# Kernel tuning notes

Hardware: AMD Instinct MI355X
Metric: run time of the kernel (lower is better)

The kernel has to match this reference:

```python
import jax, jax.numpy as jnp
import numpy as np

B, L, D_MODEL, D_MEM = 4, 8192, 512, 512
SSM_DIM = D_MODEL + D_MEM


def setup_inputs() -> dict:
    key = jax.random.key(0)
    ks = jax.random.split(key, 4)
    s = 0.02
    return {
        "x": jax.random.normal(ks[0], (B, L, D_MODEL), dtype=jnp.float32),
        "W_av": jax.random.normal(ks[1], (4 * D_MEM, D_MODEL), dtype=jnp.float32) * s,
        "b_av": jnp.zeros((4 * D_MEM,), dtype=jnp.float32),
        "W_go": jax.random.normal(ks[2], (D_MODEL, SSM_DIM), dtype=jnp.float32) * s,
        "b_go": jnp.zeros((D_MODEL,), dtype=jnp.float32),
        "W_out": jax.random.normal(ks[3], (2 * D_MODEL, D_MODEL), dtype=jnp.float32) * s,
        "b_out": jnp.zeros((2 * D_MODEL,), dtype=jnp.float32),
    }


def reference(x, W_av, b_av, W_go, b_go, W_out, b_out):
    d = D_MEM
    b = x.shape[0]
    # alpha_v = Linear(d_model -> 4*d_memory) on x[:, :-1]
    av = jnp.einsum("bld,kd->blk", x[:, :-1], W_av) + b_av
    # NRU memory update: alpha+*v+ - alpha-*v-  (all nonlins default to identity)
    ms_inp = av[..., :d] * av[..., d:2 * d] - av[..., 2 * d:3 * d] * av[..., 3 * d:4 * d]
    # associative cumsum scan along length, prefixed with zero initial memory
    ms = jnp.cumsum(ms_inp, axis=1)
    m_init = jnp.zeros((b, 1, d), dtype=x.dtype)
    ms = jnp.concatenate([m_init, ms], axis=1)  # [b, L, d_memory]
    ssm_inp = jnp.concatenate([x, ms], axis=2)  # [b, L, ssm_dim]
    # SSM sublayer (external registry module) stubbed as identity
    ssm_out = ssm_inp
    y = jnp.einsum("blk,dk->bld", ssm_out, W_go) + b_go  # gated_out
    y = jax.nn.gelu(y, approximate=False)  # activation='gelu' (torch exact erf)
    z = jnp.einsum("bld,kd->blk", y, W_out) + b_out  # [b, L, 2*d_model]
    y = z[..., :D_MODEL] * jax.nn.sigmoid(z[..., D_MODEL:])
    return y
```

## Files before the change

kernel.cpp:

```cpp
#include <hip/hip_runtime.h>
#include <hip/hip_bf16.h>
#include <math.h>

#define B_SZ 4
#define L_SZ 8192
#define DM 512
#define DMEM 512
#define M1 (B_SZ * (L_SZ - 1))
#define M2 (B_SZ * L_SZ)

typedef _Float16 h16;
typedef __attribute__((ext_vector_type(2))) _Float16 f16x2;
typedef __attribute__((ext_vector_type(8))) _Float16 f16x8;
typedef __attribute__((ext_vector_type(4))) float f32x4;

#define MFMA16(a, b, c) __builtin_amdgcn_mfma_f32_16x16x32_f16((a), (b), (c), 0, 0, 0)
#define WAVES_EU(mn, mx) __attribute__((amdgpu_waves_per_eu(mn, mx)))

__device__ __forceinline__ void gl16(const void* g, void* l) {
    __builtin_amdgcn_global_load_lds(
        (const __attribute__((address_space(1))) void*)g,
        (__attribute__((address_space(3))) void*)l, 16, 0, 0);
}

__device__ __forceinline__ f16x8 lds_frag(const h16* base, int row, int col, int key) {
    return *(const f16x8*)((const char*)base + row * 128 + ((col * 2) ^ (key << 4)));
}

__device__ __forceinline__ void xcd_remap(int& bx, int& by) {
    int gx = gridDim.x, gy = gridDim.y;
    int nwg = gx * gy;
    int lin = blockIdx.y * gx + blockIdx.x;
    int chunk = nwg >> 3;
    int l = (lin & 7) * chunk + (lin >> 3);
    by = l % gy;
    bx = l / gy;
}

__global__ __launch_bounds__(256) void prep_all(
    const float* __restrict__ x, const float* __restrict__ Wgo,
    const float* __restrict__ Wav, const float* __restrict__ Wout,
    h16* __restrict__ xh, h16* __restrict__ Wgoh,
    h16* __restrict__ Wavh, h16* __restrict__ Wouth)
{
    int i = blockIdx.x * 256 + threadIdx.x;
    const float* s;
    h16* d;
    if (i < 2097152) {
        int m = i >> 6, bb = i & 63;
        s = x + (size_t)m * 512 + bb * 8;
        d = xh + (size_t)m * 512 + (bb ^ (m & 7)) * 8;
    } else {
        int j = i - 2097152;
        if (j < 65536) {
            int r = j >> 7, bb = j & 127;
            s = Wgo + (size_t)r * 1024 + bb * 8;
            d = Wgoh + (size_t)r * 1024 + (bb ^ (r & 7)) * 8;
        } else if (j < 196608) {
            int k = j - 65536;
            int P = k >> 6, bb = k & 63;
            int by = P >> 7, lo = P & 127;
            int half = lo >> 6, g = (lo >> 4) & 3, nl = lo & 15;
            int orig = g * 512 + by * 32 + half * 16 + nl;
            s = Wav + (size_t)orig * 512 + bb * 8;
            d = Wavh + (size_t)P * 512 + (bb ^ (P & 7)) * 8;
        } else {
            int k = j - 196608;
            int P = k >> 6, bb = k & 63;
            int by = P >> 7, lo = P & 127;
            int chunk = lo >> 5, g = (lo >> 4) & 1, nl = lo & 15;
            int orig = g * 512 + by * 64 + chunk * 16 + nl;
            s = Wout + (size_t)orig * 512 + bb * 8;
            d = Wouth + (size_t)P * 512 + (bb ^ (P & 7)) * 8;
        }
    }
    const float4* sv = (const float4*)s;
    float4 v0 = sv[0], v1 = sv[1];
    float vv[8] = {v0.x, v0.y, v0.z, v0.w, v1.x, v1.y, v1.z, v1.w};
    f16x8 hh;
    #pragma unroll
    for (int j = 0; j < 8; ++j) hh[j] = (h16)vv[j];
    *(f16x8*)d = hh;
}

#define PIPE_WAIT(N) do { \
    asm volatile("s_waitcnt vmcnt(" #N ")" ::: "memory"); \
    __builtin_amdgcn_s_barrier(); \
    asm volatile("" ::: "memory"); \
} while (0)
#define PIPE_POST() do { \
    __builtin_amdgcn_s_barrier(); \
    asm volatile("" ::: "memory"); \
} while (0)

__global__ __launch_bounds__(256) WAVES_EU(4, 4) void gemm_av_mfma(
    const h16* __restrict__ xh, const h16* __restrict__ Wh,
    const float* __restrict__ bav, h16* __restrict__ ms_inp)
{
    __shared__ __align__(16) h16 As[128 * 64];
    __shared__ __align__(16) h16 Bh[128 * 64];

    int bx, by; xcd_remap(bx, by);
    const int tid = threadIdx.x, lane = tid & 63, w = tid >> 6;
    const int wm = (w & 1) * 64, wn = (w >> 1) * 64;
    const int bm = bx * 128;
    const int ln = lane & 15, ko = (lane >> 4) * 8;
    const int kb = ln & 7;
    char* lA = (char*)As; char* lH = (char*)Bh;
    const int wb = w * 1024;

    const char *aP[4], *hP[4];
    {
        const int r8 = lane >> 3, c16 = (lane & 7) * 16;
        #pragma unroll
        for (int i = 0; i < 4; ++i) {
            int row = i * 32 + w * 8 + r8;
            int mg = bm + row; if (mg > M1 - 1) mg = M1 - 1;
            size_t xr = (size_t)mg + (unsigned)mg / (L_SZ - 1);
            aP[i] = (const char*)xh + xr * (DM * 2) + c16;
            size_t br = (size_t)(by * 128 + row) * (DM * 2) + c16;
            hP[i] = (const char*)Wh + br;
        }
    }
    int ka[4];
    #pragma unroll
    for (int fm = 0; fm < 4; ++fm) {
        int m = bm + wm + fm * 16 + ln;
        int mg = m > M1 - 1 ? M1 - 1 : m;
        ka[fm] = (int)((mg + (unsigned)mg / (L_SZ - 1)) & 7);
    }

    f32x4 acc[4][4];
    #pragma unroll
    for (int i = 0; i < 4; ++i)
        #pragma unroll
        for (int j = 0; j < 4; ++j) acc[i][j] = (f32x4){0.f, 0.f, 0.f, 0.f};

#define STAGE_AV(koff) do { \
    gl16(aP[0] + (koff), lA + 0 * 4096 + wb); gl16(hP[0] + (koff), lH + 0 * 4096 + wb); \
    gl16(aP[1] + (koff), lA + 1 * 4096 + wb); gl16(hP[1] + (koff), lH + 1 * 4096 + wb); \
    gl16(aP[2] + (koff), lA + 2 * 4096 + wb); gl16(hP[2] + (koff), lH + 2 * 4096 + wb); \
    gl16(aP[3] + (koff), lA + 3 * 4096 + wb); gl16(hP[3] + (koff), lH + 3 * 4096 + wb); \
} while (0)

    STAGE_AV(0);
    for (int kt = 0; kt < 8; ++kt) {
        asm volatile("s_waitcnt vmcnt(0)" ::: "memory");
        __syncthreads();
        #pragma unroll
        for (int s = 0; s < 2; ++s) {
            const int c = s * 32 + ko;
            f16x8 a[4];
            #pragma unroll
            for (int fm = 0; fm < 4; ++fm)
                a[fm] = lds_frag(As, wm + fm * 16 + ln, c, ka[fm]);
            #pragma unroll
            for (int fn = 0; fn < 4; ++fn) {
                f16x8 vh = lds_frag(Bh, wn + fn * 16 + ln, c, kb);
                #pragma unroll
                for (int fm = 0; fm < 4; ++fm)
                    acc[fm][fn] = MFMA16(a[fm], vh, acc[fm][fn]);
            }
        }
        __syncthreads();
        if (kt < 7) STAGE_AV((kt + 1) * 128);
    }
#undef STAGE_AV

    const int lm = (lane >> 4) * 4;
    const int nn = by * 32 + (wn >> 6) * 16 + ln;
    const float b0 = bav[nn], b1 = bav[nn + 512], b2 = bav[nn + 1024], b3 = bav[nn + 1536];
    #pragma unroll
    for (int fm = 0; fm < 4; ++fm) {
        #pragma unroll
        for (int i = 0; i < 4; ++i) {
            int m = bm + wm + fm * 16 + lm + i;
            if (m < M1) {
                float a0 = acc[fm][0][i] + b0;
                float a1 = acc[fm][1][i] + b1;
                float a2 = acc[fm][2][i] + b2;
                float a3 = acc[fm][3][i] + b3;
                ms_inp[(size_t)m * DMEM + nn] = (h16)(a0 * a1 - a2 * a3);
            }
        }
    }
}

__global__ __launch_bounds__(256) void scan_pass1(
    const h16* __restrict__ ms_inp, float* __restrict__ csum)
{
    int b = blockIdx.y;
    int c = blockIdx.x * 4 + (threadIdx.x >> 6);
    int t = threadIdx.x & 63;
    int l0 = c * 32;
    int len = min(32, (L_SZ - 1) - l0);
    const h16* p = ms_inp + ((size_t)b * (L_SZ - 1) + l0) * DMEM + t * 8;
    float s[8] = {0.f, 0.f, 0.f, 0.f, 0.f, 0.f, 0.f, 0.f};
    for (int i = 0; i < len; ++i) {
        f16x8 v = *(const f16x8*)(p + (size_t)i * DMEM);
        #pragma unroll
        for (int j = 0; j < 8; ++j) s[j] += (float)v[j];
    }
    float* q = csum + ((size_t)b * 256 + c) * DMEM + t * 8;
    *(float4*)q       = make_float4(s[0], s[1], s[2], s[3]);
    *(float4*)(q + 4) = make_float4(s[4], s[5], s[6], s[7]);
}

__global__ __launch_bounds__(256) void scan_pass2(float* __restrict__ csum)
{
    __shared__ float wsum[4];
    int b = blockIdx.x >> 9, d = blockIdx.x & 511;
    int t = threadIdx.x, lane = t & 63, wv = t >> 6;
    float* p = csum + (size_t)b * 256 * DMEM + d;
    float v = p[(size_t)t * DMEM];
    #pragma unroll
    for (int off = 1; off < 64; off <<= 1) {
        float u = __shfl_up(v, off, 64);
        if (lane >= off) v += u;
    }
    if (lane == 63) wsum[wv] = v;
    __syncthreads();
    float add = 0.f;
    #pragma unroll
    for (int i = 0; i < 4; ++i) if (i < wv) add += wsum[i];
    v += add;
    float ex = __shfl_up(v, 1, 64);
    if (lane == 0) ex = add;
    p[(size_t)t * DMEM] = ex;
}

__global__ __launch_bounds__(256) void scan_pass3(
    const h16* __restrict__ ms_inp, const float* __restrict__ csum,
    h16* __restrict__ msh)
{
    int b = blockIdx.y;
    int c = blockIdx.x * 4 + (threadIdx.x >> 6);
    int t = threadIdx.x & 63;
    int l0 = c * 32;
    int len = min(32, (L_SZ - 1) - l0);
    const float* q = csum + ((size_t)b * 256 + c) * DMEM + t * 8;
    float run[8];
    #pragma unroll
    for (int j = 0; j < 8; ++j) run[j] = q[j];
    const h16* p = ms_inp + ((size_t)b * (L_SZ - 1) + l0) * DMEM + t * 8;
    if (c == 0) {
        f16x8 z = {};
        *(f16x8*)(msh + (size_t)b * L_SZ * DMEM + t * 8) = z;
    }
    for (int i = 0; i < len; ++i) {
        f16x8 v = *(const f16x8*)(p + (size_t)i * DMEM);
        f16x8 o;
        #pragma unroll
        for (int j = 0; j < 8; ++j) { run[j] += (float)v[j]; o[j] = (h16)run[j]; }
        int m = b * L_SZ + l0 + 1 + i;
        int db = t ^ (m & 7);
        *(f16x8*)(msh + (size_t)m * DMEM + db * 8) = o;
    }
}

__global__ __launch_bounds__(256) WAVES_EU(2, 2) void gemm_go_mfma(
    const h16* __restrict__ xh, const h16* __restrict__ msh,
    const h16* __restrict__ Wh,
    const float* __restrict__ bgo, h16* __restrict__ yh)
{
    __shared__ __align__(16) h16 As[2][128 * 64];
    __shared__ __align__(16) h16 Bh[2][128 * 64];

    int bx, by; xcd_remap(bx, by);
    const int tid = threadIdx.x, lane = tid & 63, w = tid >> 6;
    const int wm = (w & 1) * 64, wn = (w >> 1) * 64;
    const int bm = bx * 128, bn = by * 128;
    const int ln = lane & 15, ko = (lane >> 4) * 8;
    const int kk = ln & 7;
    const int wb = w * 1024;

    const char *xP[4], *mP[4], *hP[4];
    {
        const int r8 = lane >> 3, c16 = (lane & 7) * 16;
        #pragma unroll
        for (int i = 0; i < 4; ++i) {
            int row = i * 32 + w * 8 + r8;
            size_t ar = (size_t)(bm + row) * (DM * 2) + c16;
            xP[i] = (const char*)xh + ar;
            mP[i] = (const char*)msh + ar;
            size_t br = (size_t)(bn + row) * (2 * DM * 2) + c16;
            hP[i] = (const char*)Wh + br;
        }
    }

    f32x4 acc[4][4];
    #pragma unroll
    for (int i = 0; i < 4; ++i)
        #pragma unroll
        for (int j = 0; j < 4; ++j) acc[i][j] = (f32x4){0.f, 0.f, 0.f, 0.f};

#define STAGE_GO(tt, sel) do { \
    char* dA = (char*)As[sel]; char* dB = (char*)Bh[sel]; \
    const int bo = (tt) * 128; \
    if ((tt) < 8) { \
        const int ao = (tt) * 128; \
        gl16(xP[0] + ao, dA + 0 * 4096 + wb); gl16(hP[0] + bo, dB + 0 * 4096 + wb); \
        gl16(xP[1] + ao, dA + 1 * 4096 + wb); gl16(hP[1] + bo, dB + 1 * 4096 + wb); \
        gl16(xP[2] + ao, dA + 2 * 4096 + wb); gl16(hP[2] + bo, dB + 2 * 4096 + wb); \
        gl16(xP[3] + ao, dA + 3 * 4096 + wb); gl16(hP[3] + bo, dB + 3 * 4096 + wb); \
    } else { \
        const int ao = ((tt) - 8) * 128; \
        gl16(mP[0] + ao, dA + 0 * 4096 + wb); gl16(hP[0] + bo, dB + 0 * 4096 + wb); \
        gl16(mP[1] + ao, dA + 1 * 4096 + wb); gl16(hP[1] + bo, dB + 1 * 4096 + wb); \
        gl16(mP[2] + ao, dA + 2 * 4096 + wb); gl16(hP[2] + bo, dB + 2 * 4096 + wb); \
        gl16(mP[3] + ao, dA + 3 * 4096 + wb); gl16(hP[3] + bo, dB + 3 * 4096 + wb); \
    } \
} while (0)

    STAGE_GO(0, 0);
    STAGE_GO(1, 1);
    for (int kt = 0; kt < 16; ++kt) {
        if (kt < 15) PIPE_WAIT(8); else PIPE_WAIT(0);
        const h16* A = As[kt & 1];
        const h16* B = Bh[kt & 1];
        #pragma unroll
        for (int s = 0; s < 2; ++s) {
            const int c = s * 32 + ko;
            f16x8 a[4];
            #pragma unroll
            for (int fm = 0; fm < 4; ++fm)
                a[fm] = lds_frag(A, wm + fm * 16 + ln, c, kk);
            #pragma unroll
            for (int fn = 0; fn < 4; ++fn) {
                f16x8 vh = lds_frag(B, wn + fn * 16 + ln, c, kk);
                #pragma unroll
                for (int fm = 0; fm < 4; ++fm)
                    acc[fm][fn] = MFMA16(a[fm], vh, acc[fm][fn]);
            }
        }
        PIPE_POST();
        if (kt + 2 < 16) STAGE_GO(kt + 2, kt & 1);
    }
#undef STAGE_GO

    const int lm = (lane >> 4) * 4;
    #pragma unroll
    for (int fm = 0; fm < 4; ++fm) {
        #pragma unroll
        for (int fn = 0; fn < 4; ++fn) {
            int n = bn + wn + fn * 16 + ln;
            float bias = bgo[n];
            #pragma unroll
            for (int i = 0; i < 4; ++i) {
                int m = bm + wm + fm * 16 + lm + i;
                float t = acc[fm][fn][i] + bias;
                float g = 0.5f * t * (1.0f + erff(t * 0.70710678118654752f));
                int nsw = (((n >> 3) ^ (m & 7)) << 3) | (n & 7);
                yh[(size_t)m * DM + nsw] = (h16)g;
            }
        }
    }
}

__global__ __launch_bounds__(256) WAVES_EU(2, 2) void gemm_out_mfma(
    const h16* __restrict__ yh, const h16* __restrict__ Wh,
    const float* __restrict__ bout, float* __restrict__ out)
{
    __shared__ __align__(16) h16 As[2][128 * 64];
    __shared__ __align__(16) h16 Bh[2][128 * 64];

    int bx, by; xcd_remap(bx, by);
    const int tid = threadIdx.x, lane = tid & 63, w = tid >> 6;
    const int wm = (w & 1) * 64, wn = (w >> 1) * 64;
    const int bm = bx * 128;
    const int ln = lane & 15, ko = (lane >> 4) * 8;
    const int kk = ln & 7;
    const int wb = w * 1024;

    const char *aP[4], *hP[4];
    {
        const int r8 = lane >> 3, c16 = (lane & 7) * 16;
        #pragma unroll
        for (int i = 0; i < 4; ++i) {
            int row = i * 32 + w * 8 + r8;
            aP[i] = (const char*)yh + (size_t)(bm + row) * (DM * 2) + c16;
            size_t br = (size_t)(by * 128 + row) * (DM * 2) + c16;
            hP[i] = (const char*)Wh + br;
        }
    }

    f32x4 acc[4][4];
    #pragma unroll
    for (int i = 0; i < 4; ++i)
        #pragma unroll
        for (int j = 0; j < 4; ++j) acc[i][j] = (f32x4){0.f, 0.f, 0.f, 0.f};

#define STAGE_OUT(koff, sel) do { \
    char* dA = (char*)As[sel]; char* dB = (char*)Bh[sel]; \
    gl16(aP[0] + (koff), dA + 0 * 4096 + wb); gl16(hP[0] + (koff), dB + 0 * 4096 + wb); \
    gl16(aP[1] + (koff), dA + 1 * 4096 + wb); gl16(hP[1] + (koff), dB + 1 * 4096 + wb); \
    gl16(aP[2] + (koff), dA + 2 * 4096 + wb); gl16(hP[2] + (koff), dB + 2 * 4096 + wb); \
    gl16(aP[3] + (koff), dA + 3 * 4096 + wb); gl16(hP[3] + (koff), dB + 3 * 4096 + wb); \
} while (0)

    STAGE_OUT(0, 0);
    STAGE_OUT(128, 1);
    for (int kt = 0; kt < 8; ++kt) {
        if (kt < 7) PIPE_WAIT(8); else PIPE_WAIT(0);
        const h16* A = As[kt & 1];
        const h16* B = Bh[kt & 1];
        #pragma unroll
        for (int s = 0; s < 2; ++s) {
            const int c = s * 32 + ko;
            f16x8 a[4];
            #pragma unroll
            for (int fm = 0; fm < 4; ++fm)
                a[fm] = lds_frag(A, wm + fm * 16 + ln, c, kk);
            #pragma unroll
            for (int fn = 0; fn < 4; ++fn) {
                f16x8 vh = lds_frag(B, wn + fn * 16 + ln, c, kk);
                #pragma unroll
                for (int fm = 0; fm < 4; ++fm)
                    acc[fm][fn] = MFMA16(a[fm], vh, acc[fm][fn]);
            }
        }
        PIPE_POST();
        if (kt + 2 < 8) STAGE_OUT((kt + 2) * 128, kt & 1);
    }
#undef STAGE_OUT

    const int lm = (lane >> 4) * 4;
    #pragma unroll
    for (int fm = 0; fm < 4; ++fm) {
        #pragma unroll
        for (int cp = 0; cp < 2; ++cp) {
            int ncol = by * 64 + ((wn >> 5) + cp) * 16 + ln;
            float bz0 = bout[ncol], bz1 = bout[ncol + 512];
            #pragma unroll
            for (int i = 0; i < 4; ++i) {
                int m = bm + wm + fm * 16 + lm + i;
                float z0 = acc[fm][cp * 2 + 0][i] + bz0;
                float z1 = acc[fm][cp * 2 + 1][i] + bz1;
                out[(size_t)m * DM + ncol] = z0 * (1.0f / (1.0f + expf(-z1)));
            }
        }
    }
}

extern "C" void kernel_launch(void* const* d_in, const int* in_sizes, int n_in,
                              void* d_out, int out_size, void* d_ws, size_t ws_size,
                              hipStream_t stream)
{
    const float* x    = (const float*)d_in[0];
    const float* Wav  = (const float*)d_in[1];
    const float* bav  = (const float*)d_in[2];
    const float* Wgo  = (const float*)d_in[3];
    const float* bgo  = (const float*)d_in[4];
    const float* Wout = (const float*)d_in[5];
    const float* bout = (const float*)d_in[6];
    float* out = (float*)d_out;

    char* ws = (char*)d_ws;
    const size_t MB = 1 << 20;
    h16*   ms_inp = (h16*)ws;
    h16*   yh     = (h16*)(ws + 32 * MB);
    h16*   xh     = (h16*)(ws + 64 * MB);
    h16*   msh    = (h16*)(ws + 96 * MB);
    h16*   Wavh   = (h16*)(ws + 129 * MB);
    h16*   Wgoh   = (h16*)(ws + 131 * MB);
    h16*   Wouth  = (h16*)(ws + 132 * MB);
    float* csum   = (float*)(ws + 133 * MB);

    prep_all<<<9216, 256, 0, stream>>>(x, Wgo, Wav, Wout, xh, Wgoh, Wavh, Wouth);
    gemm_av_mfma<<<dim3(256, 16), 256, 0, stream>>>(xh, Wavh, bav, ms_inp);
    scan_pass1<<<dim3(64, B_SZ), 256, 0, stream>>>(ms_inp, csum);
    scan_pass2<<<2048, 256, 0, stream>>>(csum);
    scan_pass3<<<dim3(64, B_SZ), 256, 0, stream>>>(ms_inp, csum, msh);
    gemm_go_mfma<<<dim3(256, 4), 256, 0, stream>>>(xh, msh, Wgoh, bgo, yh);
    gemm_out_mfma<<<dim3(256, 8), 256, 0, stream>>>(yh, Wouth, bout, out);
}
```

Baseline: 233.2 us.

## Replace double-buffered LDS pipeline with single buffer and higher occupancy in GEMMs

```diff
diff --git a/kernel.cpp b/kernel.cpp
--- a/kernel.cpp
+++ b/kernel.cpp
@@ -83,16 +83,6 @@
     *(f16x8*)d = hh;
 }
 
-#define PIPE_WAIT(N) do { \
-    asm volatile("s_waitcnt vmcnt(" #N ")" ::: "memory"); \
-    __builtin_amdgcn_s_barrier(); \
-    asm volatile("" ::: "memory"); \
-} while (0)
-#define PIPE_POST() do { \
-    __builtin_amdgcn_s_barrier(); \
-    asm volatile("" ::: "memory"); \
-} while (0)
-
 __global__ __launch_bounds__(256) WAVES_EU(4, 4) void gemm_av_mfma(
     const h16* __restrict__ xh, const h16* __restrict__ Wh,
     const float* __restrict__ bav, h16* __restrict__ ms_inp)
@@ -258,13 +248,13 @@
     }
 }
 
-__global__ __launch_bounds__(256) WAVES_EU(2, 2) void gemm_go_mfma(
+__global__ __launch_bounds__(256) WAVES_EU(4, 4) void gemm_go_mfma(
     const h16* __restrict__ xh, const h16* __restrict__ msh,
     const h16* __restrict__ Wh,
     const float* __restrict__ bgo, h16* __restrict__ yh)
 {
-    __shared__ __align__(16) h16 As[2][128 * 64];
-    __shared__ __align__(16) h16 Bh[2][128 * 64];
+    __shared__ __align__(16) h16 As[128 * 64];
+    __shared__ __align__(16) h16 Bh[128 * 64];
 
     int bx, by; xcd_remap(bx, by);
     const int tid = threadIdx.x, lane = tid & 63, w = tid >> 6;
@@ -272,6 +262,7 @@
     const int bm = bx * 128, bn = by * 128;
     const int ln = lane & 15, ko = (lane >> 4) * 8;
     const int kk = ln & 7;
+    char* lA = (char*)As; char* lH = (char*)Bh;
     const int wb = w * 1024;
 
     const char *xP[4], *mP[4], *hP[4];
@@ -294,47 +285,44 @@
         #pragma unroll
         for (int j = 0; j < 4; ++j) acc[i][j] = (f32x4){0.f, 0.f, 0.f, 0.f};
 
-#define STAGE_GO(tt, sel) do { \
-    char* dA = (char*)As[sel]; char* dB = (char*)Bh[sel]; \
+#define STAGE_GO(tt) do { \
     const int bo = (tt) * 128; \
     if ((tt) < 8) { \
         const int ao = (tt) * 128; \
-        gl16(xP[0] + ao, dA + 0 * 4096 + wb); gl16(hP[0] + bo, dB + 0 * 4096 + wb); \
-        gl16(xP[1] + ao, dA + 1 * 4096 + wb); gl16(hP[1] + bo, dB + 1 * 4096 + wb); \
-        gl16(xP[2] + ao, dA + 2 * 4096 + wb); gl16(hP[2] + bo, dB + 2 * 4096 + wb); \
-        gl16(xP[3] + ao, dA + 3 * 4096 + wb); gl16(hP[3] + bo, dB + 3 * 4096 + wb); \
+        gl16(xP[0] + ao, lA + 0 * 4096 + wb); gl16(hP[0] + bo, lH + 0 * 4096 + wb); \
+        gl16(xP[1] + ao, lA + 1 * 4096 + wb); gl16(hP[1] + bo, lH + 1 * 4096 + wb); \
+        gl16(xP[2] + ao, lA + 2 * 4096 + wb); gl16(hP[2] + bo, lH + 2 * 4096 + wb); \
+        gl16(xP[3] + ao, lA + 3 * 4096 + wb); gl16(hP[3] + bo, lH + 3 * 4096 + wb); \
     } else { \
         const int ao = ((tt) - 8) * 128; \
-        gl16(mP[0] + ao, dA + 0 * 4096 + wb); gl16(hP[0] + bo, dB + 0 * 4096 + wb); \
-        gl16(mP[1] + ao, dA + 1 * 4096 + wb); gl16(hP[1] + bo, dB + 1 * 4096 + wb); \
-        gl16(mP[2] + ao, dA + 2 * 4096 + wb); gl16(hP[2] + bo, dB + 2 * 4096 + wb); \
-        gl16(mP[3] + ao, dA + 3 * 4096 + wb); gl16(hP[3] + bo, dB + 3 * 4096 + wb); \
+        gl16(mP[0] + ao, lA + 0 * 4096 + wb); gl16(hP[0] + bo, lH + 0 * 4096 + wb); \
+        gl16(mP[1] + ao, lA + 1 * 4096 + wb); gl16(hP[1] + bo, lH + 1 * 4096 + wb); \
+        gl16(mP[2] + ao, lA + 2 * 4096 + wb); gl16(hP[2] + bo, lH + 2 * 4096 + wb); \
+        gl16(mP[3] + ao, lA + 3 * 4096 + wb); gl16(hP[3] + bo, lH + 3 * 4096 + wb); \
     } \
 } while (0)
 
-    STAGE_GO(0, 0);
-    STAGE_GO(1, 1);
+    STAGE_GO(0);
     for (int kt = 0; kt < 16; ++kt) {
-        if (kt < 15) PIPE_WAIT(8); else PIPE_WAIT(0);
-        const h16* A = As[kt & 1];
-        const h16* B = Bh[kt & 1];
+        asm volatile("s_waitcnt vmcnt(0)" ::: "memory");
+        __syncthreads();
         #pragma unroll
         for (int s = 0; s < 2; ++s) {
             const int c = s * 32 + ko;
             f16x8 a[4];
             #pragma unroll
             for (int fm = 0; fm < 4; ++fm)
-                a[fm] = lds_frag(A, wm + fm * 16 + ln, c, kk);
+                a[fm] = lds_frag(As, wm + fm * 16 + ln, c, kk);
             #pragma unroll
             for (int fn = 0; fn < 4; ++fn) {
-                f16x8 vh = lds_frag(B, wn + fn * 16 + ln, c, kk);
+                f16x8 vh = lds_frag(Bh, wn + fn * 16 + ln, c, kk);
                 #pragma unroll
                 for (int fm = 0; fm < 4; ++fm)
                     acc[fm][fn] = MFMA16(a[fm], vh, acc[fm][fn]);
             }
         }
-        PIPE_POST();
-        if (kt + 2 < 16) STAGE_GO(kt + 2, kt & 1);
+        __syncthreads();
+        if (kt < 15) STAGE_GO(kt + 1);
     }
 #undef STAGE_GO
 
@@ -357,12 +345,12 @@
     }
 }
 
-__global__ __launch_bounds__(256) WAVES_EU(2, 2) void gemm_out_mfma(
+__global__ __launch_bounds__(256) WAVES_EU(4, 4) void gemm_out_mfma(
     const h16* __restrict__ yh, const h16* __restrict__ Wh,
     const float* __restrict__ bout, float* __restrict__ out)
 {
-    __shared__ __align__(16) h16 As[2][128 * 64];
-    __shared__ __align__(16) h16 Bh[2][128 * 64];
+    __shared__ __align__(16) h16 As[128 * 64];
+    __shared__ __align__(16) h16 Bh[128 * 64];
 
     int bx, by; xcd_remap(bx, by);
     const int tid = threadIdx.x, lane = tid & 63, w = tid >> 6;
@@ -370,6 +358,7 @@
     const int bm = bx * 128;
     const int ln = lane & 15, ko = (lane >> 4) * 8;
     const int kk = ln & 7;
+    char* lA = (char*)As; char* lH = (char*)Bh;
     const int wb = w * 1024;
 
     const char *aP[4], *hP[4];
@@ -390,37 +379,34 @@
         #pragma unroll
         for (int j = 0; j < 4; ++j) acc[i][j] = (f32x4){0.f, 0.f, 0.f, 0.f};
 
-#define STAGE_OUT(koff, sel) do { \
-    char* dA = (char*)As[sel]; char* dB = (char*)Bh[sel]; \
-    gl16(aP[0] + (koff), dA + 0 * 4096 + wb); gl16(hP[0] + (koff), dB + 0 * 4096 + wb); \
-    gl16(aP[1] + (koff), dA + 1 * 4096 + wb); gl16(hP[1] + (koff), dB + 1 * 4096 + wb); \
-    gl16(aP[2] + (koff), dA + 2 * 4096 + wb); gl16(hP[2] + (koff), dB + 2 * 4096 + wb); \
-    gl16(aP[3] + (koff), dA + 3 * 4096 + wb); gl16(hP[3] + (koff), dB + 3 * 4096 + wb); \
+#define STAGE_OUT(koff) do { \
+    gl16(aP[0] + (koff), lA + 0 * 4096 + wb); gl16(hP[0] + (koff), lH + 0 * 4096 + wb); \
+    gl16(aP[1] + (koff), lA + 1 * 4096 + wb); gl16(hP[1] + (koff), lH + 1 * 4096 + wb); \
+    gl16(aP[2] + (koff), lA + 2 * 4096 + wb); gl16(hP[2] + (koff), lH + 2 * 4096 + wb); \
+    gl16(aP[3] + (koff), lA + 3 * 4096 + wb); gl16(hP[3] + (koff), lH + 3 * 4096 + wb); \
 } while (0)
 
-    STAGE_OUT(0, 0);
-    STAGE_OUT(128, 1);
+    STAGE_OUT(0);
     for (int kt = 0; kt < 8; ++kt) {
-        if (kt < 7) PIPE_WAIT(8); else PIPE_WAIT(0);
-        const h16* A = As[kt & 1];
-        const h16* B = Bh[kt & 1];
+        asm volatile("s_waitcnt vmcnt(0)" ::: "memory");
+        __syncthreads();
         #pragma unroll
         for (int s = 0; s < 2; ++s) {
             const int c = s * 32 + ko;
             f16x8 a[4];
             #pragma unroll
             for (int fm = 0; fm < 4; ++fm)
-                a[fm] = lds_frag(A, wm + fm * 16 + ln, c, kk);
+                a[fm] = lds_frag(As, wm + fm * 16 + ln, c, kk);
             #pragma unroll
             for (int fn = 0; fn < 4; ++fn) {
-                f16x8 vh = lds_frag(B, wn + fn * 16 + ln, c, kk);
+                f16x8 vh = lds_frag(Bh, wn + fn * 16 + ln, c, kk);
                 #pragma unroll
                 for (int fm = 0; fm < 4; ++fm)
                     acc[fm][fn] = MFMA16(a[fm], vh, acc[fm][fn]);
             }
         }
-        PIPE_POST();
-        if (kt + 2 < 8) STAGE_OUT((kt + 2) * 128, kt & 1);
+        __syncthreads();
+        if (kt < 7) STAGE_OUT((kt + 1) * 128);
     }
 #undef STAGE_OUT
 
```

New measurement: 240.2 us. 1.03x slower.
